# Optimization experiments

Hardware: AMD Instinct MI355X
Metric: run time of the kernel (lower is better)

Reference implementation:

```python
import jax, jax.numpy as jnp
import numpy as np

BN_EPS = 1e-5
W_EPS = 1e-6


def _interp_one(tgt, src, src_feats, k):
    """tgt: (n,3), src: (m,3), src_feats: (C2,m) -> (C2,n).
    k-NN inverse-distance weighted interpolation (torch: cdist -> sort -> gather)."""
    # Squared Euclidean distances via the GEMM form (avoids (n,m,3) intermediate).
    sq = (jnp.sum(tgt * tgt, axis=1)[:, None]
          + jnp.sum(src * src, axis=1)[None, :]
          - 2.0 * (tgt @ src.T))                      # (n, m)
    d = jnp.sqrt(jnp.maximum(sq, 1e-12))
    neg_d, idx = jax.lax.top_k(-d, k)                 # k smallest distances
    dk = -neg_d                                        # (n, k)
    w = 1.0 / (dk + W_EPS)
    w = w / jnp.sum(w, axis=1, keepdims=True)          # (n, k)
    sel = src_feats[:, idx]                            # (C2, n, k) gather
    return jnp.sum(sel * w[None, :, :], axis=2)        # (C2, n)


def reference(tgt, src, tgt_feats, src_feats, W, gamma, beta, k):
    # Per-batch kNN interpolation of image features onto cloud points.
    interp = jax.vmap(_interp_one, in_axes=(0, 0, 0, None))(tgt, src, src_feats, k)  # (B, C2, n)
    feats = jnp.concatenate([interp, tgt_feats], axis=1)  # (B, C2+C1, n)
    B, C, n = feats.shape
    # torch cat(dim=2) of per-batch (1,C,n) slices -> (1, C, B*n)
    x = feats.transpose(1, 0, 2).reshape(C, B * n)[None, :, :]
    # SharedMLP block: 1x1 Conv1d (no bias) + BatchNorm1d (training stats) + ReLU
    y = jnp.einsum('oc,bcn->bon', W, x)                # (1, 512, B*n)
    mean = jnp.mean(y, axis=(0, 2), keepdims=True)
    var = jnp.mean((y - mean) ** 2, axis=(0, 2), keepdims=True)
    y = (y - mean) / jnp.sqrt(var + BN_EPS)
    y = y * gamma[None, :, None] + beta[None, :, None]
    return jax.nn.relu(y)


def setup_inputs() -> dict:
    key = jax.random.key(0)
    ks = jax.random.split(key, 6)
    B, n, m, C1, C2 = 2, 16384, 4096, 512, 384
    out_ch = 512
    tgt = jax.random.normal(ks[0], (B, n, 3), dtype=jnp.float32) * 10.0
    src = jax.random.normal(ks[1], (B, m, 3), dtype=jnp.float32) * 10.0
    tgt_feats = jax.random.normal(ks[2], (B, C1, n), dtype=jnp.float32)
    src_feats = jax.random.normal(ks[3], (B, C2, m), dtype=jnp.float32)
    W = jax.random.normal(ks[4], (out_ch, C1 + C2), dtype=jnp.float32) * 0.02
    gamma = jnp.ones((out_ch,), dtype=jnp.float32)
    beta = jnp.zeros((out_ch,), dtype=jnp.float32)
    return {"tgt": tgt, "src": src, "tgt_feats": tgt_feats, "src_feats": src_feats,
            "W": W, "gamma": gamma, "beta": beta, "k": 3}
```

## Files before the change

kernel.cpp:

```cpp
#include <hip/hip_runtime.h>

#define NTGT 16384
#define MSRC 4096
#define BB   2
#define C1D  512
#define C2D  384
#define KDIM 896
#define OCH  512
#define NCOL 32768

typedef short   short8   __attribute__((ext_vector_type(8)));
typedef float   floatx16 __attribute__((ext_vector_type(16)));

static __device__ __forceinline__ unsigned short f2bf(float f) {
    union { float f; unsigned u; } v; v.f = f;
    unsigned r = (v.u + 0x7fffu + ((v.u >> 16) & 1u)) >> 16;
    return (unsigned short)r;
}

__global__ __launch_bounds__(256) void knn_scan(const float* __restrict__ tgt,
                                                const float* __restrict__ src,
                                                float* __restrict__ part_m,
                                                int* __restrict__ part_id) {
    __shared__ float4 s_pts[2048];
    const int t = threadIdx.x;
    const int g = blockIdx.x >> 1;
    const int h = blockIdx.x & 1;
    const int colbase = g * 64;
    const int b = colbase >> 14;
    const int lane = t & 63;
    const int q = t >> 6;

    const float* sb = src + (size_t)b * (MSRC * 3) + h * (2048 * 3);
    #pragma unroll
    for (int k = 0; k < 8; ++k) {
        int p = k * 256 + t;
        float x = sb[p * 3 + 0], y = sb[p * 3 + 1], z = sb[p * 3 + 2];
        s_pts[p] = make_float4(x, y, z, x * x + y * y + z * z);
    }
    __syncthreads();

    const int col = colbase + lane;
    const float tx = tgt[(size_t)col * 3 + 0];
    const float ty = tgt[(size_t)col * 3 + 1];
    const float tz = tgt[(size_t)col * 3 + 2];
    const float tx2 = -2.0f * tx, ty2 = -2.0f * ty, tz2 = -2.0f * tz;

    const int jbase = q * 512;

    int k0 = 0x7fffffff, k1 = 0x7fffffff, k2 = 0x7fffffff, k3 = 0x7fffffff, k4 = 0x7fffffff;
    for (int cc = 0; cc < 64; ++cc) {
        const float4* P = &s_pts[jbase + cc * 8];
        float4 p0 = P[0], p1 = P[1], p2 = P[2], p3 = P[3];
        float4 p4 = P[4], p5 = P[5], p6 = P[6], p7 = P[7];
        float m0 = fmaf(p0.x, tx2, fmaf(p0.y, ty2, fmaf(p0.z, tz2, p0.w)));
        float m1 = fmaf(p1.x, tx2, fmaf(p1.y, ty2, fmaf(p1.z, tz2, p1.w)));
        float m2 = fmaf(p2.x, tx2, fmaf(p2.y, ty2, fmaf(p2.z, tz2, p2.w)));
        float m3 = fmaf(p3.x, tx2, fmaf(p3.y, ty2, fmaf(p3.z, tz2, p3.w)));
        float m4 = fmaf(p4.x, tx2, fmaf(p4.y, ty2, fmaf(p4.z, tz2, p4.w)));
        float m5 = fmaf(p5.x, tx2, fmaf(p5.y, ty2, fmaf(p5.z, tz2, p5.w)));
        float m6 = fmaf(p6.x, tx2, fmaf(p6.y, ty2, fmaf(p6.z, tz2, p6.w)));
        float m7 = fmaf(p7.x, tx2, fmaf(p7.y, ty2, fmaf(p7.z, tz2, p7.w)));
        float cm = fminf(fminf(fminf(m0, m1), fminf(m2, m3)),
                         fminf(fminf(m4, m5), fminf(m6, m7)));
        int key = ((int)(cm * 1024.0f) << 6) | cc;
        int x = key, tt;
        tt = min(k0, x); x = max(k0, x); k0 = tt;
        tt = min(k1, x); x = max(k1, x); k1 = tt;
        tt = min(k2, x); x = max(k2, x); k2 = tt;
        tt = min(k3, x); x = max(k3, x); k3 = tt;
        k4 = min(k4, x);
    }

    float b0 = 3.4e38f, b1 = 3.4e38f, b2 = 3.4e38f, b3 = 3.4e38f, b4 = 3.4e38f;
    int   i0 = 0x7fffffff, i1 = 0x7fffffff, i2 = 0x7fffffff, i3 = 0x7fffffff, i4 = 0x7fffffff;
    int cids[5] = { k0 & 63, k1 & 63, k2 & 63, k3 & 63, k4 & 63 };
    #pragma unroll
    for (int s = 0; s < 5; ++s) {
        int base = jbase + cids[s] * 8;
        #pragma unroll
        for (int r = 0; r < 8; ++r) {
            float4 P = s_pts[base + r];
            float m = fmaf(P.x, tx2, fmaf(P.y, ty2, fmaf(P.z, tz2, P.w)));
            int j = base + r;
            if (m < b4) {
                if (m < b3) { b4 = b3; i4 = i3;
                    if (m < b2) { b3 = b2; i3 = i2;
                        if (m < b1) { b2 = b1; i2 = i1;
                            if (m < b0) { b1 = b0; i1 = i0; b0 = m; i0 = j; }
                            else        { b1 = m; i1 = j; }
                        } else { b2 = m; i2 = j; }
                    } else { b3 = m; i3 = j; }
                } else { b4 = m; i4 = j; }
            }
        }
    }

    __syncthreads();
    float* s_m = (float*)s_pts;
    int*   s_i = (int*)(s_m + 1280);
    s_m[t * 5 + 0] = b0; s_m[t * 5 + 1] = b1; s_m[t * 5 + 2] = b2; s_m[t * 5 + 3] = b3; s_m[t * 5 + 4] = b4;
    s_i[t * 5 + 0] = i0; s_i[t * 5 + 1] = i1; s_i[t * 5 + 2] = i2; s_i[t * 5 + 3] = i3; s_i[t * 5 + 4] = i4;
    __syncthreads();

    if (t < 64) {
        float m0 = 3.4e38f, m1 = 3.4e38f, m2 = 3.4e38f, m3 = 3.4e38f, m4 = 3.4e38f;
        int   g0 = 0x7fffffff, g1 = 0x7fffffff, g2 = 0x7fffffff, g3 = 0x7fffffff, g4 = 0x7fffffff;
        #pragma unroll
        for (int qq = 0; qq < 4; ++qq) {
            int row = qq * 64 + t;
            #pragma unroll
            for (int s = 0; s < 5; ++s) {
                float d = s_m[row * 5 + s]; int di = s_i[row * 5 + s];
                bool lt4 = (d < m4) || (d == m4 && di < g4);
                if (lt4) {
                    bool lt3 = (d < m3) || (d == m3 && di < g3);
                    if (lt3) { m4 = m3; g4 = g3;
                        bool lt2 = (d < m2) || (d == m2 && di < g2);
                        if (lt2) { m3 = m2; g3 = g2;
                            bool lt1 = (d < m1) || (d == m1 && di < g1);
                            if (lt1) { m2 = m1; g2 = g1;
                                bool lt0 = (d < m0) || (d == m0 && di < g0);
                                if (lt0) { m1 = m0; g1 = g0; m0 = d; g0 = di; }
                                else     { m1 = d; g1 = di; }
                            } else { m2 = d; g2 = di; }
                        } else { m3 = d; g3 = di; }
                    } else { m4 = d; g4 = di; }
                }
            }
        }
        int base = ((colbase + t) * 2 + h) * 5;
        part_m[base + 0] = m0; part_m[base + 1] = m1; part_m[base + 2] = m2; part_m[base + 3] = m3; part_m[base + 4] = m4;
        int off = h * 2048;
        part_id[base + 0] = off + g0; part_id[base + 1] = off + g1; part_id[base + 2] = off + g2;
        part_id[base + 3] = off + g3; part_id[base + 4] = off + g4;
    }
}

__global__ __launch_bounds__(256) void knn_finalize(const float* __restrict__ tgt,
                                                    const float* __restrict__ src,
                                                    const float* __restrict__ part_m,
                                                    const int* __restrict__ part_id,
                                                    int* __restrict__ out_idx,
                                                    float* __restrict__ out_w) {
    const int col = blockIdx.x * 256 + threadIdx.x;
    const int b = col >> 14;
    float m0 = 3.4e38f, m1 = 3.4e38f, m2 = 3.4e38f, m3 = 3.4e38f, m4 = 3.4e38f;
    int   g0 = 0x7fffffff, g1 = 0x7fffffff, g2 = 0x7fffffff, g3 = 0x7fffffff, g4 = 0x7fffffff;
    #pragma unroll
    for (int s = 0; s < 10; ++s) {
        float d = part_m[col * 10 + s]; int di = part_id[col * 10 + s];
        bool lt4 = (d < m4) || (d == m4 && di < g4);
        if (lt4) {
            bool lt3 = (d < m3) || (d == m3 && di < g3);
            if (lt3) { m4 = m3; g4 = g3;
                bool lt2 = (d < m2) || (d == m2 && di < g2);
                if (lt2) { m3 = m2; g3 = g2;
                    bool lt1 = (d < m1) || (d == m1 && di < g1);
                    if (lt1) { m2 = m1; g2 = g1;
                        bool lt0 = (d < m0) || (d == m0 && di < g0);
                        if (lt0) { m1 = m0; g1 = g0; m0 = d; g0 = di; }
                        else     { m1 = d; g1 = di; }
                    } else { m2 = d; g2 = di; }
                } else { m3 = d; g3 = di; }
            } else { m4 = d; g4 = di; }
        }
    }
    const double txd = (double)tgt[(size_t)col * 3 + 0];
    const double tyd = (double)tgt[(size_t)col * 3 + 1];
    const double tzd = (double)tgt[(size_t)col * 3 + 2];
    double a0 = 1e300, a1 = 1e300, a2 = 1e300;
    int    f0 = 0x7fffffff, f1 = 0x7fffffff, f2 = 0x7fffffff;
    int cand[5] = { g0, g1, g2, g3, g4 };
    #pragma unroll
    for (int s = 0; s < 5; ++s) {
        int id = cand[s];
        const float* sp = src + (size_t)b * (MSRC * 3) + (size_t)id * 3;
        double dx = (double)sp[0] - txd, dy = (double)sp[1] - tyd, dz = (double)sp[2] - tzd;
        double d = dx * dx + dy * dy + dz * dz;
        bool lt2c = (d < a2) || (d == a2 && id < f2);
        if (lt2c) {
            bool lt1c = (d < a1) || (d == a1 && id < f1);
            if (lt1c) { a2 = a1; f2 = f1;
                bool lt0c = (d < a0) || (d == a0 && id < f0);
                if (lt0c) { a1 = a0; f1 = f0; a0 = d; f0 = id; }
                else      { a1 = d; f1 = id; }
            } else { a2 = d; f2 = id; }
        }
    }
    double d0 = sqrt(fmax(a0, 1e-12)), d1 = sqrt(fmax(a1, 1e-12)), d2 = sqrt(fmax(a2, 1e-12));
    double w0 = 1.0 / (d0 + 1e-6), w1 = 1.0 / (d1 + 1e-6), w2 = 1.0 / (d2 + 1e-6);
    double ws = w0 + w1 + w2;
    out_idx[col * 3 + 0] = f0; out_idx[col * 3 + 1] = f1; out_idx[col * 3 + 2] = f2;
    out_w[col * 3 + 0] = (float)(w0 / ws);
    out_w[col * 3 + 1] = (float)(w1 / ws);
    out_w[col * 3 + 2] = (float)(w2 / ws);
}

__global__ __launch_bounds__(256) void wcast_kernel(const float* __restrict__ W,
                                                    unsigned short* __restrict__ Wb) {
    for (int e = blockIdx.x * 256 + threadIdx.x; e < OCH * KDIM; e += gridDim.x * 256)
        Wb[e] = f2bf(W[e]);
}

__global__ __launch_bounds__(256) void interp_kernel(const float* __restrict__ src_feats,
                                                     const int* __restrict__ knn_idx,
                                                     const float* __restrict__ knn_w,
                                                     unsigned short* __restrict__ X) {
    __shared__ float rows[4][4096];
    const int t = threadIdx.x;
    const int cchunk = blockIdx.x % 96;
    const int colchunk = blockIdx.x / 96;
    const int colbase = colchunk * 4096;
    const int b = colbase >> 14;
    const int rbase = cchunk * 4;
    #pragma unroll
    for (int r = 0; r < 4; ++r) {
        const float* sp = src_feats + (size_t)(b * C2D + rbase + r) * MSRC;
        #pragma unroll
        for (int u = 0; u < 4; ++u) {
            int e = (u * 256 + t) * 4;
            *(float4*)&rows[r][e] = *(const float4*)&sp[e];
        }
    }
    __syncthreads();
    for (int u = 0; u < 16; ++u) {
        int col = colbase + u * 256 + t;
        int i0 = knn_idx[col * 3 + 0], i1 = knn_idx[col * 3 + 1], i2 = knn_idx[col * 3 + 2];
        float w0 = knn_w[col * 3 + 0], w1 = knn_w[col * 3 + 1], w2 = knn_w[col * 3 + 2];
        #pragma unroll
        for (int r = 0; r < 4; ++r) {
            float v = w0 * rows[r][i0] + w1 * rows[r][i1] + w2 * rows[r][i2];
            X[(size_t)(rbase + r) * NCOL + col] = f2bf(v);
        }
    }
}

__global__ __launch_bounds__(256) void tgtcopy_kernel(const float* __restrict__ tgt_feats,
                                                      unsigned short* __restrict__ X) {
    const int total = C1D * NCOL / 4;
    for (int e = blockIdx.x * 256 + threadIdx.x; e < total; e += gridDim.x * 256) {
        int c1 = e >> 13;
        int within = e & 8191;
        int col = within * 4;
        int b = col >> 14;
        int i = col & 16383;
        float4 v = *(const float4*)&tgt_feats[(size_t)(b * C1D + c1) * NTGT + i];
        ushort4 o;
        o.x = f2bf(v.x); o.y = f2bf(v.y); o.z = f2bf(v.z); o.w = f2bf(v.w);
        *(ushort4*)&X[(size_t)(C2D + c1) * NCOL + col] = o;
    }
}

__global__ __launch_bounds__(256) void gemm_kernel(const unsigned short* __restrict__ Wb,
                                                   const unsigned short* __restrict__ X,
                                                   float* __restrict__ Y) {
    __shared__ short    As[512][40];
    __shared__ unsigned Bs[64][20];
    const int t = threadIdx.x;
    const int nbase = blockIdx.x * 64;
    const int lane = t & 63;
    const int w = t >> 6;
    const int mwave = w * 128;
    const int l31 = lane & 31;
    const int lh = lane >> 5;
    const int k2 = t >> 4;
    const int ng = t & 15;

    floatx16 acc[4][2];
    #pragma unroll
    for (int mt = 0; mt < 4; ++mt)
        #pragma unroll
        for (int nt = 0; nt < 2; ++nt)
            acc[mt][nt] = (floatx16)(0.0f);

    for (int kb = 0; kb < 28; ++kb) {
        const int kbase = kb * 32;
        __syncthreads();
        #pragma unroll
        for (int u = 0; u < 8; ++u) {
            int s = u * 256 + t;
            int row = s >> 2, ko = s & 3;
            *(int4*)&As[row][ko * 8] = *(const int4*)&Wb[(size_t)row * KDIM + kbase + ko * 8];
        }
        {
            ushort4 r0 = *(const ushort4*)&X[(size_t)(kbase + 2 * k2 + 0) * NCOL + nbase + ng * 4];
            ushort4 r1 = *(const ushort4*)&X[(size_t)(kbase + 2 * k2 + 1) * NCOL + nbase + ng * 4];
            Bs[ng * 4 + 0][k2] = (unsigned)r0.x | ((unsigned)r1.x << 16);
            Bs[ng * 4 + 1][k2] = (unsigned)r0.y | ((unsigned)r1.y << 16);
            Bs[ng * 4 + 2][k2] = (unsigned)r0.z | ((unsigned)r1.z << 16);
            Bs[ng * 4 + 3][k2] = (unsigned)r0.w | ((unsigned)r1.w << 16);
        }
        __syncthreads();
        #pragma unroll
        for (int kk = 0; kk < 2; ++kk) {
            short8 b0 = *(const short8*)&Bs[l31][kk * 8 + lh * 4];
            short8 b1 = *(const short8*)&Bs[32 + l31][kk * 8 + lh * 4];
            #pragma unroll
            for (int mt = 0; mt < 4; ++mt) {
                short8 a = *(const short8*)&As[mwave + mt * 32 + l31][kk * 16 + lh * 8];
                acc[mt][0] = __builtin_amdgcn_mfma_f32_32x32x16_bf16(a, b0, acc[mt][0], 0, 0, 0);
                acc[mt][1] = __builtin_amdgcn_mfma_f32_32x32x16_bf16(a, b1, acc[mt][1], 0, 0, 0);
            }
        }
    }
    #pragma unroll
    for (int mt = 0; mt < 4; ++mt)
        #pragma unroll
        for (int nt = 0; nt < 2; ++nt)
            #pragma unroll
            for (int r = 0; r < 16; ++r) {
                int row = mwave + mt * 32 + 4 * lh + (r & 3) + 8 * (r >> 2);
                int colo = nbase + nt * 32 + l31;
                Y[(size_t)row * NCOL + colo] = acc[mt][nt][r];
            }
}

__global__ __launch_bounds__(256) void reduce_kernel(const float* __restrict__ Y,
                                                     float* __restrict__ stats,
                                                     const float* __restrict__ gamma,
                                                     const float* __restrict__ beta) {
    __shared__ float ss[256], sq[256];
    const int o = blockIdx.x, t = threadIdx.x;
    const float* row = Y + (size_t)o * NCOL;
    float s = 0.f, s2 = 0.f;
    #pragma unroll 4
    for (int u = 0; u < 32; ++u) {
        float4 v = *(const float4*)&row[(u * 256 + t) * 4];
        s  += v.x + v.y + v.z + v.w;
        s2 += v.x * v.x + v.y * v.y + v.z * v.z + v.w * v.w;
    }
    ss[t] = s; sq[t] = s2;
    __syncthreads();
    for (int st = 128; st > 0; st >>= 1) {
        if (t < st) { ss[t] += ss[t + st]; sq[t] += sq[t + st]; }
        __syncthreads();
    }
    if (t == 0) {
        float mean = ss[0] * (1.0f / NCOL);
        float var  = sq[0] * (1.0f / NCOL) - mean * mean;
        float inv  = 1.0f / sqrtf(var + 1e-5f);
        float sc   = gamma[o] * inv;
        stats[o]       = sc;
        stats[OCH + o] = beta[o] - mean * sc;
    }
}

__global__ __launch_bounds__(256) void bn_kernel(float* __restrict__ Y,
                                                 const float* __restrict__ stats) {
    const int total = OCH * NCOL / 4;
    for (int e = blockIdx.x * 256 + threadIdx.x; e < total; e += gridDim.x * 256) {
        int o = e >> 13;
        float sc = stats[o];
        float sh = stats[OCH + o];
        float4 v = *(float4*)&Y[(size_t)e * 4];
        v.x = fmaxf(v.x * sc + sh, 0.f);
        v.y = fmaxf(v.y * sc + sh, 0.f);
        v.z = fmaxf(v.z * sc + sh, 0.f);
        v.w = fmaxf(v.w * sc + sh, 0.f);
        *(float4*)&Y[(size_t)e * 4] = v;
    }
}

extern "C" void kernel_launch(void* const* d_in, const int* in_sizes, int n_in,
                              void* d_out, int out_size, void* d_ws, size_t ws_size,
                              hipStream_t stream) {
    const float* tgt       = (const float*)d_in[0];
    const float* src       = (const float*)d_in[1];
    const float* tgt_feats = (const float*)d_in[2];
    const float* src_feats = (const float*)d_in[3];
    const float* W         = (const float*)d_in[4];
    const float* gamma     = (const float*)d_in[5];
    const float* beta      = (const float*)d_in[6];

    char* ws = (char*)d_ws;
    int*            knn_idx = (int*)(ws + 0);
    float*          knn_w   = (float*)(ws + 393216);
    unsigned short* Wb      = (unsigned short*)(ws + 786432);
    unsigned short* X       = (unsigned short*)(ws + 1703936);
    float*          stats   = (float*)(ws + 60424192);
    float*          part_m  = (float*)(ws + 1703936);
    int*            part_id = (int*)(ws + 1703936 + 1310720);
    float*          Y       = (float*)d_out;

    knn_scan<<<1024, 256, 0, stream>>>(tgt, src, part_m, part_id);
    knn_finalize<<<128, 256, 0, stream>>>(tgt, src, part_m, part_id, knn_idx, knn_w);
    wcast_kernel<<<448, 256, 0, stream>>>(W, Wb);
    interp_kernel<<<768, 256, 0, stream>>>(src_feats, knn_idx, knn_w, X);
    tgtcopy_kernel<<<2048, 256, 0, stream>>>(tgt_feats, X);
    gemm_kernel<<<512, 256, 0, stream>>>(Wb, X, Y);
    reduce_kernel<<<512, 256, 0, stream>>>(Y, stats, gamma, beta);
    bn_kernel<<<2048, 256, 0, stream>>>(Y, stats);
}
```

Measured before the change: 283.5 us.

## Fuse tgt_feats bf16 conversion into GEMM and add register prefetch

Removes the separate tgtcopy kernel. The GEMM now reads tgt_feats fp32 directly for the K rows past the 384 interpolated channels and converts them to bf16 on the fly. Global loads for the next K-block of A and B are prefetched into registers while the current block's MFMAs run. The B shared-memory tile is transposed to [k][n] so it takes one vectorized store, with a strided 4-load read per fragment instead. This drops a write and re-read of a 32 MB bf16 buffer, but doubles the B-operand read bytes in the GEMM and adds register pressure.

```diff
diff --git a/kernel.cpp b/kernel.cpp
--- a/kernel.cpp
+++ b/kernel.cpp
@@ -206,7 +206,7 @@
 __global__ __launch_bounds__(256) void interp_kernel(const float* __restrict__ src_feats,
                                                      const int* __restrict__ knn_idx,
                                                      const float* __restrict__ knn_w,
-                                                     unsigned short* __restrict__ X) {
+                                                     unsigned short* __restrict__ Xi) {
     __shared__ float rows[4][4096];
     const int t = threadIdx.x;
     const int cchunk = blockIdx.x % 96;
@@ -231,32 +231,17 @@
         #pragma unroll
         for (int r = 0; r < 4; ++r) {
             float v = w0 * rows[r][i0] + w1 * rows[r][i1] + w2 * rows[r][i2];
-            X[(size_t)(rbase + r) * NCOL + col] = f2bf(v);
-        }
-    }
-}
-
-__global__ __launch_bounds__(256) void tgtcopy_kernel(const float* __restrict__ tgt_feats,
-                                                      unsigned short* __restrict__ X) {
-    const int total = C1D * NCOL / 4;
-    for (int e = blockIdx.x * 256 + threadIdx.x; e < total; e += gridDim.x * 256) {
-        int c1 = e >> 13;
-        int within = e & 8191;
-        int col = within * 4;
-        int b = col >> 14;
-        int i = col & 16383;
-        float4 v = *(const float4*)&tgt_feats[(size_t)(b * C1D + c1) * NTGT + i];
-        ushort4 o;
-        o.x = f2bf(v.x); o.y = f2bf(v.y); o.z = f2bf(v.z); o.w = f2bf(v.w);
-        *(ushort4*)&X[(size_t)(C2D + c1) * NCOL + col] = o;
-    }
-}
-
-__global__ __launch_bounds__(256) void gemm_kernel(const unsigned short* __restrict__ Wb,
-                                                   const unsigned short* __restrict__ X,
-                                                   float* __restrict__ Y) {
+            Xi[(size_t)(rbase + r) * NCOL + col] = f2bf(v);
+        }
+    }
+}
+
+__global__ __launch_bounds__(256) void gemm2_kernel(const unsigned short* __restrict__ Wb,
+                                                    const unsigned short* __restrict__ Xi,
+                                                    const float* __restrict__ tgt_feats,
+                                                    float* __restrict__ Y) {
     __shared__ short    As[512][40];
-    __shared__ unsigned Bs[64][20];
+    __shared__ unsigned Bs[16][68];
     const int t = threadIdx.x;
     const int nbase = blockIdx.x * 64;
     const int lane = t & 63;
@@ -267,6 +252,15 @@
     const int k2 = t >> 4;
     const int ng = t & 15;
 
+    const int arow = t >> 2;
+    const int ako  = t & 3;
+    const unsigned short* Abase = Wb + (size_t)arow * KDIM + ako * 8;
+
+    const int colb = nbase + ng * 4;
+    const int bb = colb >> 14;
+    const int ii = colb & 16383;
+    const float* tf = tgt_feats + (size_t)bb * C1D * NTGT + ii;
+
     floatx16 acc[4][2];
     #pragma unroll
     for (int mt = 0; mt < 4; ++mt)
@@ -274,33 +268,64 @@
         for (int nt = 0; nt < 2; ++nt)
             acc[mt][nt] = (floatx16)(0.0f);
 
+    int4    apf[8];
+    ushort4 px0, px1;
+    float4  pf0, pf1;
+
+    #pragma unroll
+    for (int u = 0; u < 8; ++u)
+        apf[u] = *(const int4*)(Abase + (size_t)u * 64 * KDIM);
+    px0 = *(const ushort4*)&Xi[(size_t)(2 * k2 + 0) * NCOL + colb];
+    px1 = *(const ushort4*)&Xi[(size_t)(2 * k2 + 1) * NCOL + colb];
+
     for (int kb = 0; kb < 28; ++kb) {
-        const int kbase = kb * 32;
         __syncthreads();
         #pragma unroll
-        for (int u = 0; u < 8; ++u) {
-            int s = u * 256 + t;
-            int row = s >> 2, ko = s & 3;
-            *(int4*)&As[row][ko * 8] = *(const int4*)&Wb[(size_t)row * KDIM + kbase + ko * 8];
-        }
+        for (int u = 0; u < 8; ++u)
+            *(int4*)&As[u * 64 + arow][ako * 8] = apf[u];
         {
-            ushort4 r0 = *(const ushort4*)&X[(size_t)(kbase + 2 * k2 + 0) * NCOL + nbase + ng * 4];
-            ushort4 r1 = *(const ushort4*)&X[(size_t)(kbase + 2 * k2 + 1) * NCOL + nbase + ng * 4];
-            Bs[ng * 4 + 0][k2] = (unsigned)r0.x | ((unsigned)r1.x << 16);
-            Bs[ng * 4 + 1][k2] = (unsigned)r0.y | ((unsigned)r1.y << 16);
-            Bs[ng * 4 + 2][k2] = (unsigned)r0.z | ((unsigned)r1.z << 16);
-            Bs[ng * 4 + 3][k2] = (unsigned)r0.w | ((unsigned)r1.w << 16);
+            uint4 bw;
+            if (kb < 12) {
+                bw.x = (unsigned)px0.x | ((unsigned)px1.x << 16);
+                bw.y = (unsigned)px0.y | ((unsigned)px1.y << 16);
+                bw.z = (unsigned)px0.z | ((unsigned)px1.z << 16);
+                bw.w = (unsigned)px0.w | ((unsigned)px1.w << 16);
+            } else {
+                bw.x = (unsigned)f2bf(pf0.x) | ((unsigned)f2bf(pf1.x) << 16);
+                bw.y = (unsigned)f2bf(pf0.y) | ((unsigned)f2bf(pf1.y) << 16);
+                bw.z = (unsigned)f2bf(pf0.z) | ((unsigned)f2bf(pf1.z) << 16);
+                bw.w = (unsigned)f2bf(pf0.w) | ((unsigned)f2bf(pf1.w) << 16);
+            }
+            *(uint4*)&Bs[k2][ng * 4] = bw;
         }
         __syncthreads();
+        if (kb < 27) {
+            const int kn = (kb + 1) * 32;
+            #pragma unroll
+            for (int u = 0; u < 8; ++u)
+                apf[u] = *(const int4*)(Abase + (size_t)u * 64 * KDIM + kn);
+            if (kb + 1 < 12) {
+                px0 = *(const ushort4*)&Xi[(size_t)(kn + 2 * k2 + 0) * NCOL + colb];
+                px1 = *(const ushort4*)&Xi[(size_t)(kn + 2 * k2 + 1) * NCOL + colb];
+            } else {
+                const int c1 = kn - C2D + 2 * k2;
+                pf0 = *(const float4*)&tf[(size_t)(c1 + 0) * NTGT];
+                pf1 = *(const float4*)&tf[(size_t)(c1 + 1) * NTGT];
+            }
+        }
         #pragma unroll
         for (int kk = 0; kk < 2; ++kk) {
-            short8 b0 = *(const short8*)&Bs[l31][kk * 8 + lh * 4];
-            short8 b1 = *(const short8*)&Bs[32 + l31][kk * 8 + lh * 4];
+            union { uint4 u; short8 s; } bf0, bf1;
+            const int rb = kk * 8 + lh * 4;
+            bf0.u.x = Bs[rb + 0][l31];      bf1.u.x = Bs[rb + 0][32 + l31];
+            bf0.u.y = Bs[rb + 1][l31];      bf1.u.y = Bs[rb + 1][32 + l31];
+            bf0.u.z = Bs[rb + 2][l31];      bf1.u.z = Bs[rb + 2][32 + l31];
+            bf0.u.w = Bs[rb + 3][l31];      bf1.u.w = Bs[rb + 3][32 + l31];
             #pragma unroll
             for (int mt = 0; mt < 4; ++mt) {
                 short8 a = *(const short8*)&As[mwave + mt * 32 + l31][kk * 16 + lh * 8];
-                acc[mt][0] = __builtin_amdgcn_mfma_f32_32x32x16_bf16(a, b0, acc[mt][0], 0, 0, 0);
-                acc[mt][1] = __builtin_amdgcn_mfma_f32_32x32x16_bf16(a, b1, acc[mt][1], 0, 0, 0);
+                acc[mt][0] = __builtin_amdgcn_mfma_f32_32x32x16_bf16(a, bf0.s, acc[mt][0], 0, 0, 0);
+                acc[mt][1] = __builtin_amdgcn_mfma_f32_32x32x16_bf16(a, bf1.s, acc[mt][1], 0, 0, 0);
             }
         }
     }
@@ -377,7 +402,7 @@
     int*            knn_idx = (int*)(ws + 0);
     float*          knn_w   = (float*)(ws + 393216);
     unsigned short* Wb      = (unsigned short*)(ws + 786432);
-    unsigned short* X       = (unsigned short*)(ws + 1703936);
+    unsigned short* Xi      = (unsigned short*)(ws + 1703936);
     float*          stats   = (float*)(ws + 60424192);
     float*          part_m  = (float*)(ws + 1703936);
     int*            part_id = (int*)(ws + 1703936 + 1310720);
@@ -386,9 +411,8 @@
     knn_scan<<<1024, 256, 0, stream>>>(tgt, src, part_m, part_id);
     knn_finalize<<<128, 256, 0, stream>>>(tgt, src, part_m, part_id, knn_idx, knn_w);
     wcast_kernel<<<448, 256, 0, stream>>>(W, Wb);
-    interp_kernel<<<768, 256, 0, stream>>>(src_feats, knn_idx, knn_w, X);
-    tgtcopy_kernel<<<2048, 256, 0, stream>>>(tgt_feats, X);
-    gemm_kernel<<<512, 256, 0, stream>>>(Wb, X, Y);
+    interp_kernel<<<768, 256, 0, stream>>>(src_feats, knn_idx, knn_w, Xi);
+    gemm2_kernel<<<512, 256, 0, stream>>>(Wb, Xi, tgt_feats, Y);
     reduce_kernel<<<512, 256, 0, stream>>>(Y, stats, gamma, beta);
     bn_kernel<<<2048, 256, 0, stream>>>(Y, stats);
 }
```

Result: slower. 377.6 us (+33.2%).
